# Performance work log

Measured on AMD Instinct MI355X. Metric: run time of the kernel, lower is better.

The kernel has to match this reference:

```python
import jax, jax.numpy as jnp
import numpy as np

B, C, N, K, O = 8, 64, 4096, 20, 64
EPS = 1e-5


def setup_inputs() -> dict:
    key = jax.random.key(0)
    k1, k2, k3 = jax.random.split(key, 3)
    x = jax.random.normal(k1, (B, C, N), dtype=jnp.float32)
    # Conv2d(2C, O, kernel_size=1) -> weight [O, 2C], bias [O]
    fan_in = 2 * C
    bound = 1.0 / np.sqrt(fan_in)
    W = jax.random.uniform(k2, (O, 2 * C), minval=-bound, maxval=bound, dtype=jnp.float32)
    b = jax.random.uniform(k3, (O,), minval=-bound, maxval=bound, dtype=jnp.float32)
    gamma = jnp.ones((O,), dtype=jnp.float32)
    beta = jnp.zeros((O,), dtype=jnp.float32)
    return {"x": x, "W": W, "b": b, "gamma": gamma, "beta": beta}


def reference(x, W, b, gamma, beta):
    k = K
    Bs, Cs, Ns = x.shape
    x_t = jnp.transpose(x, (0, 2, 1))  # [B, N, C]
    # pairwise squared distances (monotonic with cdist, same topk indices)
    sq = jnp.sum(x_t * x_t, axis=-1)  # [B, N]
    d2 = sq[:, :, None] + sq[:, None, :] - 2.0 * jnp.einsum("bnc,bmc->bnm", x_t, x_t)
    valid_k = min(k, Ns - 1)
    _, idx = jax.lax.top_k(-d2, valid_k + 1)  # smallest distances
    idx = idx[:, :, 1:]  # drop self -> [B, N, k]
    # gather neighbor features per batch
    nbr = jax.vmap(lambda xt, i: xt[i])(x_t, idx)  # [B, N, k, C]
    central = x_t[:, :, None, :]  # [B, N, 1, C]
    edge = jnp.concatenate(
        [jnp.broadcast_to(central, (Bs, Ns, k, Cs)), nbr - central], axis=-1
    )  # [B, N, k, 2C]
    # 1x1 conv == channel matmul
    y = jnp.einsum("bnkc,oc->bonk", edge, W) + b[None, :, None, None]  # [B, O, N, k]
    # BatchNorm2d in training mode: batch statistics over (B, N, k)
    mean = jnp.mean(y, axis=(0, 2, 3), keepdims=True)
    var = jnp.var(y, axis=(0, 2, 3), keepdims=True)
    yn = (y - mean) * jax.lax.rsqrt(var + EPS)
    yn = gamma[None, :, None, None] * yn + beta[None, :, None, None]
    out = jax.nn.relu(yn)
    return jnp.max(out, axis=-1)  # [B, O, N]
```

## Files before the change

kernel.cpp:

```cpp
#include <hip/hip_runtime.h>
#include <hip/hip_bf16.h>

#define BB 8
#define CC 64
#define NN 4096
#define KK 20
#define OO 64
#define FMAXV 3.402823466e38f

typedef __attribute__((ext_vector_type(8))) short short8;
typedef __attribute__((ext_vector_type(4))) float f32x4;

__global__ __launch_bounds__(256) void ktrans(const float* __restrict__ x,
                                              float* __restrict__ xt,
                                              unsigned short* __restrict__ xb,
                                              float* __restrict__ sq) {
  __shared__ float tile[64][65];
  const int b = blockIdx.y, n0 = blockIdx.x * 64;
  const int lane = threadIdx.x & 63, grp = threadIdx.x >> 6;
  #pragma unroll
  for (int j = 0; j < 16; ++j) {
    int c = grp + j * 4;
    tile[c][lane] = x[((size_t)b * CC + c) * NN + n0 + lane];
  }
  __syncthreads();
  #pragma unroll
  for (int j = 0; j < 16; ++j) {
    int n = grp + j * 4;
    float vv = tile[lane][n];
    size_t off = ((size_t)b * NN + n0 + n) * CC + lane;
    xt[off] = vv;
    unsigned int u = __builtin_bit_cast(unsigned int, vv);
    xb[off] = (unsigned short)((u + 0x7FFFu + ((u >> 16) & 1u)) >> 16);
  }
  if (threadIdx.x < 64) {
    float s = 0.f;
    #pragma unroll
    for (int c = 0; c < 64; ++c) { float vv = tile[c][lane]; s += vv * vv; }
    sq[(size_t)b * NN + lane + n0] = s;
  }
}

__device__ __forceinline__ int lanes_below(unsigned long long m) {
  unsigned lo = (unsigned)m, hi = (unsigned)(m >> 32);
  int c = __builtin_amdgcn_mbcnt_lo(lo, 0);
  return (int)__builtin_amdgcn_mbcnt_hi(hi, (unsigned)c);
}

__device__ __forceinline__ unsigned packkey(float d, int m) {
  unsigned u = __builtin_bit_cast(unsigned, d);
  u ^= ((int)u < 0) ? 0xFFFFFFFFu : 0x80000000u;
  return (u & 0xFFFFF000u) | (unsigned)m;
}

__device__ __forceinline__ float unpackkey(unsigned t) {
  unsigned u = t | 0xFFFu;
  u = (u & 0x80000000u) ? (u ^ 0x80000000u) : ~u;
  return __builtin_bit_cast(float, u);
}

__device__ __forceinline__ unsigned bitonic64(unsigned v, int lane) {
  #pragma unroll
  for (int k = 2; k <= 64; k <<= 1) {
    #pragma unroll
    for (int j = k >> 1; j >= 1; j >>= 1) {
      unsigned o = (unsigned)__shfl_xor((int)v, j);
      bool up    = ((lane & k) == 0);
      bool lower = ((lane & j) == 0);
      unsigned mn = (v < o) ? v : o;
      unsigned mx = (v < o) ? o : v;
      v = (up == lower) ? mn : mx;
    }
  }
  return v;
}

__global__ __launch_bounds__(256, 4) void kknn6(const unsigned short* __restrict__ xb,
                                                const float* __restrict__ sq,
                                                unsigned* __restrict__ kcand) {
  __shared__ unsigned slist[4][16][32];
  __shared__ unsigned sbuf[4][16][64];
  const int lane = threadIdx.x & 63, w = threadIdx.x >> 6;
  const int wid = blockIdx.x * 4 + w;
  const int b = wid >> 9;
  const int half = (wid >> 8) & 1;
  const int n0g = (wid & 255) * 16;
  const int ch0 = half * (NN / 2);
  const int l15 = lane & 15, q = lane >> 4;
  const unsigned long long qmask = 0xFFFFull << (q * 16);

  const unsigned short* xbB = xb + (size_t)b * NN * CC;
  const float* sqB = sq + (size_t)b * NN;

  #pragma unroll
  for (int i = 0; i < 8; ++i) {
    int idx = i * 64 + lane;
    slist[w][idx >> 5][idx & 31] = 0xFFFFFFFFu;
  }

  short8 afr[2];
  #pragma unroll
  for (int ks = 0; ks < 2; ++ks)
    afr[ks] = __builtin_bit_cast(short8, *(const int4*)(xbB + (size_t)(n0g + l15) * CC + ks * 32 + q * 8));

  float tauf4[4];
  int cnt4[4], done4[4];
  #pragma unroll
  for (int j = 0; j < 4; ++j) { tauf4[j] = FMAXV; cnt4[j] = 0; done4[j] = 0; }

  for (int t = 0; t < 32; ++t) {
    const int cb = ch0 + t * 64;
    short8 bfr[4][2];
    float sv[4];
    #pragma unroll
    for (int ct = 0; ct < 4; ++ct) {
      #pragma unroll
      for (int ks = 0; ks < 2; ++ks)
        bfr[ct][ks] = __builtin_bit_cast(short8,
            *(const int4*)(xbB + (size_t)(cb + ct * 16 + l15) * CC + ks * 32 + q * 8));
      sv[ct] = sqB[cb + ct * 16 + l15];
    }
    f32x4 acc[4];
    #pragma unroll
    for (int ct = 0; ct < 4; ++ct) {
      acc[ct] = (f32x4){0.f, 0.f, 0.f, 0.f};
      acc[ct] = __builtin_amdgcn_mfma_f32_16x16x32_bf16(afr[0], bfr[ct][0], acc[ct], 0, 0, 0);
      acc[ct] = __builtin_amdgcn_mfma_f32_16x16x32_bf16(afr[1], bfr[ct][1], acc[ct], 0, 0, 0);
    }

    #pragma unroll
    for (int ct = 0; ct < 4; ++ct) {
      const int colg = cb + ct * 16 + l15;
      float dj[4];
      bool pj[4];
      #pragma unroll
      for (int j = 0; j < 4; ++j) {
        float d = sv[ct] - 2.f * acc[ct][j];
        if (colg == n0g + q * 4 + j) d = FMAXV;
        dj[j] = d;
        pj[j] = d <= tauf4[j];
      }
      if (!__ballot(pj[0] | pj[1] | pj[2] | pj[3])) continue;
      #pragma unroll
      for (int j = 0; j < 4; ++j) {
        unsigned long long bal = __ballot(pj[j]);
        if (!bal) continue;
        const int rowl = q * 4 + j;
        int posq = lanes_below(bal & qmask);
        if (pj[j]) sbuf[w][rowl][(cnt4[j] + posq) & 63] = packkey(dj[j], colg);
        cnt4[j] += __popcll(bal & qmask);
        unsigned long long mb = __ballot(cnt4[j] - done4[j] >= 32);
        while (mb) {
          int src = __ffsll(mb) - 1;
          int qm = src >> 4;
          int rowm = qm * 4 + j;
          int dsrc = __shfl(done4[j], src);
          unsigned v = (lane < 32) ? slist[w][rowm][lane]
                                   : sbuf[w][rowm][(dsrc + lane - 32) & 63];
          v = bitonic64(v, lane);
          if (lane < 32) slist[w][rowm][lane] = v;
          unsigned tn = (unsigned)__shfl((int)v, 31);
          if (q == qm) { tauf4[j] = unpackkey(tn); done4[j] += 32; }
          mb &= ~(0xFFFFull << (qm * 16));
        }
      }
    }
  }

  #pragma unroll
  for (int j = 0; j < 4; ++j) {
    unsigned long long mb = __ballot(cnt4[j] > done4[j]);
    while (mb) {
      int src = __ffsll(mb) - 1;
      int qm = src >> 4;
      int rowm = qm * 4 + j;
      int dsrc = __shfl(done4[j], src);
      int csrc = __shfl(cnt4[j], src);
      int rem = csrc - dsrc;
      unsigned v = (lane < 32) ? slist[w][rowm][lane]
                 : ((lane - 32) < rem ? sbuf[w][rowm][(dsrc + lane - 32) & 63] : 0xFFFFFFFFu);
      v = bitonic64(v, lane);
      if (lane < 32) slist[w][rowm][lane] = v;
      if (q == qm) done4[j] = cnt4[j];
      mb &= ~(0xFFFFull << (qm * 16));
    }
  }

  unsigned* kc = kcand + (((size_t)b * 2 + half) * NN + n0g) * 32;
  #pragma unroll
  for (int i = 0; i < 8; ++i) {
    int idx = i * 64 + lane;
    kc[idx] = slist[w][idx >> 5][idx & 31];
  }
}

__global__ __launch_bounds__(256) void kmerge(const unsigned* __restrict__ kcand,
                                              const float* __restrict__ xt,
                                              const float* __restrict__ sq,
                                              int* __restrict__ knn) {
  const int lane = threadIdx.x & 63, w = threadIdx.x >> 6;
  const int gw = blockIdx.x * 4 + w;
  const int hl = lane & 31;

  for (int it = 0; it < 2; ++it) {
    const int rbase = gw * 4 + it * 2;
    const int b = rbase >> 12;
    const int n = rbase & (NN - 1);

    const unsigned* kc0 = kcand + (((size_t)b * 2 + 0) * NN) * 32;
    const unsigned* kc1 = kcand + (((size_t)b * 2 + 1) * NN) * 32;
    unsigned vA = (lane < 32) ? kc0[(size_t)n * 32 + lane] : kc1[(size_t)n * 32 + (lane - 32)];
    vA = bitonic64(vA, lane);
    unsigned vB = (lane < 32) ? kc0[(size_t)(n + 1) * 32 + lane] : kc1[(size_t)(n + 1) * 32 + (lane - 32)];
    vB = bitonic64(vB, lane);
    unsigned kx = (unsigned)__shfl_xor((int)vB, 32);
    unsigned key = (lane < 32) ? vA : kx;
    int m = (int)(key & 0xFFFu);
    const int rowg = n + ((lane >= 32) ? 1 : 0);

    const float* xtB = xt + (size_t)b * NN * CC;
    const float* sqB = sq + (size_t)b * NN;
    const float4* pr = (const float4*)(xtB + (size_t)rowg * CC);
    const float4* pm = (const float4*)(xtB + (size_t)m * CC);
    float s0 = 0.f, s1 = 0.f, s2 = 0.f, s3 = 0.f;
    #pragma unroll
    for (int i = 0; i < 16; ++i) {
      float4 a = pr[i], c = pm[i];
      s0 += a.x * c.x; s1 += a.y * c.y; s2 += a.z * c.z; s3 += a.w * c.w;
    }
    float ev = sqB[m] - 2.f * ((s0 + s1) + (s2 + s3));

    #pragma unroll
    for (int k = 2; k <= 32; k <<= 1) {
      #pragma unroll
      for (int jj = k >> 1; jj >= 1; jj >>= 1) {
        float e2 = __shfl_xor(ev, jj);
        int   m2 = __shfl_xor(m, jj);
        bool up    = ((hl & k) == 0);
        bool lower = ((hl & jj) == 0);
        bool less  = (e2 < ev) || (e2 == ev && m2 < m);
        bool take  = (up == lower) ? less : !less;
        if (take) { ev = e2; m = m2; }
      }
    }
    if (hl < KK)
      knn[((size_t)b * NN + rowg) * KK + hl] = m;
  }
}

__global__ __launch_bounds__(256) void kuv(const float* __restrict__ xt,
                                           const float* __restrict__ W,
                                           const float* __restrict__ bias,
                                           float* __restrict__ u,
                                           float* __restrict__ v) {
  __shared__ float sx[64][65];
  const int b = blockIdx.y, n0 = blockIdx.x * 64;
  const int lane = threadIdx.x & 63, w = threadIdx.x >> 6;
  const float4* src = (const float4*)(xt + ((size_t)b * NN + n0) * CC);
  for (int i = threadIdx.x; i < 1024; i += 256) {
    float4 qv = src[i];
    int nl = i >> 4, c4 = (i & 15) << 2;
    sx[nl][c4] = qv.x; sx[nl][c4+1] = qv.y; sx[nl][c4+2] = qv.z; sx[nl][c4+3] = qv.w;
  }
  const int o = lane;
  float w2r[64], wdr[64];
  const float4* W4 = (const float4*)W;
  #pragma unroll
  for (int c4 = 0; c4 < 16; ++c4) {
    float4 q1 = W4[o * 32 + c4];
    float4 q2 = W4[o * 32 + 16 + c4];
    w2r[c4*4]=q2.x; w2r[c4*4+1]=q2.y; w2r[c4*4+2]=q2.z; w2r[c4*4+3]=q2.w;
    wdr[c4*4]=q1.x-q2.x; wdr[c4*4+1]=q1.y-q2.y; wdr[c4*4+2]=q1.z-q2.z; wdr[c4*4+3]=q1.w-q2.w;
  }
  const float bo = bias[o];
  __syncthreads();
  for (int j = 0; j < 16; ++j) {
    int nl = w * 16 + j;
    float du = 0.f, dv = 0.f;
    #pragma unroll
    for (int c = 0; c < 64; ++c) {
      float xv = sx[nl][c];
      du += w2r[c] * xv;
      dv += wdr[c] * xv;
    }
    size_t off = ((size_t)b * NN + n0 + nl) * OO + o;
    u[off] = du;
    v[off] = dv + bo;
  }
}

__global__ __launch_bounds__(256) void kstats(const float* __restrict__ u,
                                              const float* __restrict__ v,
                                              const int* __restrict__ knn,
                                              float* __restrict__ umax,
                                              float* __restrict__ umin,
                                              float* __restrict__ gS) {
  const int w = threadIdx.x >> 6, lane = threadIdx.x & 63;
  const int gw = blockIdx.x * 4 + w;
  float s1 = 0.f, s2 = 0.f;
  for (int it = 0; it < 16; ++it) {
    int pair = gw * 16 + it;
    const int* ip = knn + (size_t)pair * KK;
    float vv = v[(size_t)pair * OO + lane];
    size_t ubase = ((size_t)(pair >> 12)) * NN * OO;
    float mx = -FMAXV, mn = FMAXV;
    #pragma unroll
    for (int k = 0; k < KK; ++k) {
      int id = ip[k];
      float uu = u[ubase + (size_t)id * OO + lane];
      float y = vv + uu;
      s1 += y; s2 += y * y;
      mx = fmaxf(mx, uu); mn = fminf(mn, uu);
    }
    umax[(size_t)pair * OO + lane] = mx;
    umin[(size_t)pair * OO + lane] = mn;
  }
  __shared__ float r1[4][64], r2[4][64];
  r1[w][lane] = s1; r2[w][lane] = s2;
  __syncthreads();
  if (w == 0) {
    float a = r1[0][lane] + r1[1][lane] + r1[2][lane] + r1[3][lane];
    float c = r2[0][lane] + r2[1][lane] + r2[2][lane] + r2[3][lane];
    atomicAdd(&gS[lane], a);
    atomicAdd(&gS[64 + lane], c);
  }
}

__global__ __launch_bounds__(256) void kout(const float* __restrict__ v,
                                            const float* __restrict__ umax,
                                            const float* __restrict__ umin,
                                            const float* __restrict__ gS,
                                            const float* __restrict__ gamma,
                                            const float* __restrict__ beta,
                                            float* __restrict__ out) {
  __shared__ float sA[64], sB[64];
  __shared__ float zt[64][65];
  const int b = blockIdx.y, n0 = blockIdx.x * 64;
  const int lane = threadIdx.x & 63, w = threadIdx.x >> 6;
  if (threadIdx.x < 64) {
    const float cnt = (float)BB * NN * KK;
    float m  = gS[lane] / cnt;
    float var = gS[64 + lane] / cnt - m * m;
    float A = gamma[lane] * rsqrtf(var + 1e-5f);
    sA[lane] = A;
    sB[lane] = beta[lane] - A * m;
  }
  __syncthreads();
  for (int j = 0; j < 16; ++j) {
    int nl = w * 16 + j;
    size_t off = ((size_t)b * NN + n0 + nl) * OO + lane;
    float A = sA[lane];
    float c0 = A * v[off] + sB[lane];
    float z = c0 + A * ((A > 0.f) ? umax[off] : umin[off]);
    zt[nl][lane] = fmaxf(z, 0.f);
  }
  __syncthreads();
  for (int j = 0; j < 16; ++j) {
    int o = w * 16 + j;
    out[((size_t)b * OO + o) * NN + n0 + lane] = zt[lane][o];
  }
}

extern "C" void kernel_launch(void* const* d_in, const int* in_sizes, int n_in,
                              void* d_out, int out_size, void* d_ws, size_t ws_size,
                              hipStream_t stream) {
  const float* x     = (const float*)d_in[0];
  const float* W     = (const float*)d_in[1];
  const float* bias  = (const float*)d_in[2];
  const float* gamma = (const float*)d_in[3];
  const float* beta  = (const float*)d_in[4];
  float* out = (float*)d_out;

  float* xt  = (float*)d_ws;
  float* sq  = xt  + (size_t)BB*NN*CC;
  float* u   = sq  + (size_t)BB*NN;
  float* v   = u   + (size_t)BB*NN*OO;
  float* umx = v   + (size_t)BB*NN*OO;
  float* umn = umx + (size_t)BB*NN*OO;
  float* gS  = umn + (size_t)BB*NN*OO;
  int*   knn = (int*)(gS + 128);
  unsigned short* xb = (unsigned short*)(knn + (size_t)BB*NN*KK);
  unsigned* kcand = (unsigned*)(xb + (size_t)BB*NN*CC);

  hipMemsetAsync(gS, 0, 128 * sizeof(float), stream);
  ktrans<<<dim3(NN/64, BB), 256, 0, stream>>>(x, xt, xb, sq);
  kuv   <<<dim3(NN/64, BB), 256, 0, stream>>>(xt, W, bias, u, v);
  kknn6 <<<dim3(1024),      256, 0, stream>>>(xb, sq, kcand);
  kmerge<<<dim3(2048),      256, 0, stream>>>(kcand, xt, sq, knn);
  kstats<<<dim3(512),       256, 0, stream>>>(u, v, knn, umx, umn, gS);
  kout  <<<dim3(NN/64, BB), 256, 0, stream>>>(v, umx, umn, gS, gamma, beta, out);
}
```

Baseline: 440.0 us.

## Fuse transpose with u/v projection and merge with stats; halve KNN rows per wave

```diff
diff --git a/kernel.cpp b/kernel.cpp
--- a/kernel.cpp
+++ b/kernel.cpp
@@ -11,10 +11,14 @@
 typedef __attribute__((ext_vector_type(8))) short short8;
 typedef __attribute__((ext_vector_type(4))) float f32x4;
 
-__global__ __launch_bounds__(256) void ktrans(const float* __restrict__ x,
-                                              float* __restrict__ xt,
-                                              unsigned short* __restrict__ xb,
-                                              float* __restrict__ sq) {
+__global__ __launch_bounds__(256) void kprep(const float* __restrict__ x,
+                                             const float* __restrict__ W,
+                                             const float* __restrict__ bias,
+                                             float* __restrict__ xt,
+                                             unsigned short* __restrict__ xb,
+                                             float* __restrict__ sq,
+                                             float* __restrict__ u,
+                                             float* __restrict__ v) {
   __shared__ float tile[64][65];
   const int b = blockIdx.y, n0 = blockIdx.x * 64;
   const int lane = threadIdx.x & 63, grp = threadIdx.x >> 6;
@@ -23,6 +27,16 @@
     int c = grp + j * 4;
     tile[c][lane] = x[((size_t)b * CC + c) * NN + n0 + lane];
   }
+  float w2r[64], wdr[64];
+  const float4* W4 = (const float4*)W;
+  #pragma unroll
+  for (int c4 = 0; c4 < 16; ++c4) {
+    float4 q1 = W4[lane * 32 + c4];
+    float4 q2 = W4[lane * 32 + 16 + c4];
+    w2r[c4*4]=q2.x; w2r[c4*4+1]=q2.y; w2r[c4*4+2]=q2.z; w2r[c4*4+3]=q2.w;
+    wdr[c4*4]=q1.x-q2.x; wdr[c4*4+1]=q1.y-q2.y; wdr[c4*4+2]=q1.z-q2.z; wdr[c4*4+3]=q1.w-q2.w;
+  }
+  const float bo = bias[lane];
   __syncthreads();
   #pragma unroll
   for (int j = 0; j < 16; ++j) {
@@ -30,14 +44,27 @@
     float vv = tile[lane][n];
     size_t off = ((size_t)b * NN + n0 + n) * CC + lane;
     xt[off] = vv;
-    unsigned int u = __builtin_bit_cast(unsigned int, vv);
-    xb[off] = (unsigned short)((u + 0x7FFFu + ((u >> 16) & 1u)) >> 16);
+    unsigned int uu = __builtin_bit_cast(unsigned int, vv);
+    xb[off] = (unsigned short)((uu + 0x7FFFu + ((uu >> 16) & 1u)) >> 16);
   }
   if (threadIdx.x < 64) {
     float s = 0.f;
     #pragma unroll
     for (int c = 0; c < 64; ++c) { float vv = tile[c][lane]; s += vv * vv; }
-    sq[(size_t)b * NN + lane + n0] = s;
+    sq[(size_t)b * NN + n0 + lane] = s;
+  }
+  for (int j = 0; j < 16; ++j) {
+    int nl = grp * 16 + j;
+    float du = 0.f, dv = 0.f;
+    #pragma unroll
+    for (int c = 0; c < 64; ++c) {
+      float xv = tile[c][nl];
+      du += w2r[c] * xv;
+      dv += wdr[c] * xv;
+    }
+    size_t off = ((size_t)b * NN + n0 + nl) * OO + lane;
+    u[off] = du;
+    v[off] = dv + bo;
   }
 }
 
@@ -75,25 +102,26 @@
   return v;
 }
 
-__global__ __launch_bounds__(256, 4) void kknn6(const unsigned short* __restrict__ xb,
+__global__ __launch_bounds__(256, 4) void kknn7(const unsigned short* __restrict__ xb,
                                                 const float* __restrict__ sq,
                                                 unsigned* __restrict__ kcand) {
-  __shared__ unsigned slist[4][16][32];
-  __shared__ unsigned sbuf[4][16][64];
+  __shared__ unsigned slist[4][8][32];
+  __shared__ unsigned sbuf[4][8][64];
   const int lane = threadIdx.x & 63, w = threadIdx.x >> 6;
   const int wid = blockIdx.x * 4 + w;
-  const int b = wid >> 9;
-  const int half = (wid >> 8) & 1;
-  const int n0g = (wid & 255) * 16;
+  const int b = wid >> 10;
+  const int half = (wid >> 9) & 1;
+  const int n0g = (wid & 511) * 8;
   const int ch0 = half * (NN / 2);
   const int l15 = lane & 15, q = lane >> 4;
+  const bool qlo = (q < 2);
   const unsigned long long qmask = 0xFFFFull << (q * 16);
 
   const unsigned short* xbB = xb + (size_t)b * NN * CC;
   const float* sqB = sq + (size_t)b * NN;
 
   #pragma unroll
-  for (int i = 0; i < 8; ++i) {
+  for (int i = 0; i < 4; ++i) {
     int idx = i * 64 + lane;
     slist[w][idx >> 5][idx & 31] = 0xFFFFFFFFu;
   }
@@ -101,7 +129,8 @@
   short8 afr[2];
   #pragma unroll
   for (int ks = 0; ks < 2; ++ks)
-    afr[ks] = __builtin_bit_cast(short8, *(const int4*)(xbB + (size_t)(n0g + l15) * CC + ks * 32 + q * 8));
+    afr[ks] = __builtin_bit_cast(short8,
+        *(const int4*)(xbB + (size_t)(n0g + (l15 & 7)) * CC + ks * 32 + q * 8));
 
   float tauf4[4];
   int cnt4[4], done4[4];
@@ -136,9 +165,9 @@
       #pragma unroll
       for (int j = 0; j < 4; ++j) {
         float d = sv[ct] - 2.f * acc[ct][j];
-        if (colg == n0g + q * 4 + j) d = FMAXV;
+        if (colg == n0g + ((q * 4 + j) & 7)) d = FMAXV;
         dj[j] = d;
-        pj[j] = d <= tauf4[j];
+        pj[j] = qlo && (d <= tauf4[j]);
       }
       if (!__ballot(pj[0] | pj[1] | pj[2] | pj[3])) continue;
       #pragma unroll
@@ -188,19 +217,24 @@
 
   unsigned* kc = kcand + (((size_t)b * 2 + half) * NN + n0g) * 32;
   #pragma unroll
-  for (int i = 0; i < 8; ++i) {
+  for (int i = 0; i < 4; ++i) {
     int idx = i * 64 + lane;
     kc[idx] = slist[w][idx >> 5][idx & 31];
   }
 }
 
-__global__ __launch_bounds__(256) void kmerge(const unsigned* __restrict__ kcand,
-                                              const float* __restrict__ xt,
-                                              const float* __restrict__ sq,
-                                              int* __restrict__ knn) {
+__global__ __launch_bounds__(256) void kpost(const unsigned* __restrict__ kcand,
+                                             const float* __restrict__ xt,
+                                             const float* __restrict__ sq,
+                                             const float* __restrict__ u,
+                                             const float* __restrict__ v,
+                                             float* __restrict__ umax,
+                                             float* __restrict__ umin,
+                                             float* __restrict__ gS) {
   const int lane = threadIdx.x & 63, w = threadIdx.x >> 6;
   const int gw = blockIdx.x * 4 + w;
   const int hl = lane & 31;
+  float s1 = 0.f, s2 = 0.f;
 
   for (int it = 0; it < 2; ++it) {
     const int rbase = gw * 4 + it * 2;
@@ -222,13 +256,13 @@
     const float* sqB = sq + (size_t)b * NN;
     const float4* pr = (const float4*)(xtB + (size_t)rowg * CC);
     const float4* pm = (const float4*)(xtB + (size_t)m * CC);
-    float s0 = 0.f, s1 = 0.f, s2 = 0.f, s3 = 0.f;
+    float t0 = 0.f, t1 = 0.f, t2 = 0.f, t3 = 0.f;
     #pragma unroll
     for (int i = 0; i < 16; ++i) {
       float4 a = pr[i], c = pm[i];
-      s0 += a.x * c.x; s1 += a.y * c.y; s2 += a.z * c.z; s3 += a.w * c.w;
-    }
-    float ev = sqB[m] - 2.f * ((s0 + s1) + (s2 + s3));
+      t0 += a.x * c.x; t1 += a.y * c.y; t2 += a.z * c.z; t3 += a.w * c.w;
+    }
+    float ev = sqB[m] - 2.f * ((t0 + t1) + (t2 + t3));
 
     #pragma unroll
     for (int k = 2; k <= 32; k <<= 1) {
@@ -243,86 +277,35 @@
         if (take) { ev = e2; m = m2; }
       }
     }
-    if (hl < KK)
-      knn[((size_t)b * NN + rowg) * KK + hl] = m;
-  }
-}
-
-__global__ __launch_bounds__(256) void kuv(const float* __restrict__ xt,
-                                           const float* __restrict__ W,
-                                           const float* __restrict__ bias,
-                                           float* __restrict__ u,
-                                           float* __restrict__ v) {
-  __shared__ float sx[64][65];
-  const int b = blockIdx.y, n0 = blockIdx.x * 64;
-  const int lane = threadIdx.x & 63, w = threadIdx.x >> 6;
-  const float4* src = (const float4*)(xt + ((size_t)b * NN + n0) * CC);
-  for (int i = threadIdx.x; i < 1024; i += 256) {
-    float4 qv = src[i];
-    int nl = i >> 4, c4 = (i & 15) << 2;
-    sx[nl][c4] = qv.x; sx[nl][c4+1] = qv.y; sx[nl][c4+2] = qv.z; sx[nl][c4+3] = qv.w;
-  }
-  const int o = lane;
-  float w2r[64], wdr[64];
-  const float4* W4 = (const float4*)W;
-  #pragma unroll
-  for (int c4 = 0; c4 < 16; ++c4) {
-    float4 q1 = W4[o * 32 + c4];
-    float4 q2 = W4[o * 32 + 16 + c4];
-    w2r[c4*4]=q2.x; w2r[c4*4+1]=q2.y; w2r[c4*4+2]=q2.z; w2r[c4*4+3]=q2.w;
-    wdr[c4*4]=q1.x-q2.x; wdr[c4*4+1]=q1.y-q2.y; wdr[c4*4+2]=q1.z-q2.z; wdr[c4*4+3]=q1.w-q2.w;
-  }
-  const float bo = bias[o];
-  __syncthreads();
-  for (int j = 0; j < 16; ++j) {
-    int nl = w * 16 + j;
-    float du = 0.f, dv = 0.f;
-    #pragma unroll
-    for (int c = 0; c < 64; ++c) {
-      float xv = sx[nl][c];
-      du += w2r[c] * xv;
-      dv += wdr[c] * xv;
-    }
-    size_t off = ((size_t)b * NN + n0 + nl) * OO + o;
-    u[off] = du;
-    v[off] = dv + bo;
-  }
-}
-
-__global__ __launch_bounds__(256) void kstats(const float* __restrict__ u,
-                                              const float* __restrict__ v,
-                                              const int* __restrict__ knn,
-                                              float* __restrict__ umax,
-                                              float* __restrict__ umin,
-                                              float* __restrict__ gS) {
-  const int w = threadIdx.x >> 6, lane = threadIdx.x & 63;
-  const int gw = blockIdx.x * 4 + w;
-  float s1 = 0.f, s2 = 0.f;
-  for (int it = 0; it < 16; ++it) {
-    int pair = gw * 16 + it;
-    const int* ip = knn + (size_t)pair * KK;
-    float vv = v[(size_t)pair * OO + lane];
-    size_t ubase = ((size_t)(pair >> 12)) * NN * OO;
-    float mx = -FMAXV, mn = FMAXV;
-    #pragma unroll
-    for (int k = 0; k < KK; ++k) {
-      int id = ip[k];
-      float uu = u[ubase + (size_t)id * OO + lane];
-      float y = vv + uu;
-      s1 += y; s2 += y * y;
-      mx = fmaxf(mx, uu); mn = fminf(mn, uu);
-    }
-    umax[(size_t)pair * OO + lane] = mx;
-    umin[(size_t)pair * OO + lane] = mn;
-  }
+
+    const float* uB = u + (size_t)b * NN * OO;
+    #pragma unroll
+    for (int rr = 0; rr < 2; ++rr) {
+      const int rown = n + rr;
+      float vv = v[((size_t)b * NN + rown) * OO + lane];
+      float mx = -FMAXV, mn = FMAXV;
+      #pragma unroll
+      for (int k = 0; k < KK; ++k) {
+        int id = __shfl(m, rr * 32 + k);
+        float uu = uB[(size_t)id * OO + lane];
+        float y = vv + uu;
+        s1 += y; s2 += y * y;
+        mx = fmaxf(mx, uu); mn = fminf(mn, uu);
+      }
+      umax[((size_t)b * NN + rown) * OO + lane] = mx;
+      umin[((size_t)b * NN + rown) * OO + lane] = mn;
+    }
+  }
+
   __shared__ float r1[4][64], r2[4][64];
   r1[w][lane] = s1; r2[w][lane] = s2;
   __syncthreads();
   if (w == 0) {
     float a = r1[0][lane] + r1[1][lane] + r1[2][lane] + r1[3][lane];
     float c = r2[0][lane] + r2[1][lane] + r2[2][lane] + r2[3][lane];
-    atomicAdd(&gS[lane], a);
-    atomicAdd(&gS[64 + lane], c);
+    float* g = gS + (blockIdx.x & 7) * 128;
+    atomicAdd(&g[lane], a);
+    atomicAdd(&g[64 + lane], c);
   }
 }
 
@@ -338,9 +321,15 @@
   const int b = blockIdx.y, n0 = blockIdx.x * 64;
   const int lane = threadIdx.x & 63, w = threadIdx.x >> 6;
   if (threadIdx.x < 64) {
+    float s1 = 0.f, s2 = 0.f;
+    #pragma unroll
+    for (int rsub = 0; rsub < 8; ++rsub) {
+      s1 += gS[rsub * 128 + lane];
+      s2 += gS[rsub * 128 + 64 + lane];
+    }
     const float cnt = (float)BB * NN * KK;
-    float m  = gS[lane] / cnt;
-    float var = gS[64 + lane] / cnt - m * m;
+    float m  = s1 / cnt;
+    float var = s2 / cnt - m * m;
     float A = gamma[lane] * rsqrtf(var + 1e-5f);
     sA[lane] = A;
     sB[lane] = beta[lane] - A * m;
@@ -378,15 +367,12 @@
   float* umx = v   + (size_t)BB*NN*OO;
   float* umn = umx + (size_t)BB*NN*OO;
   float* gS  = umn + (size_t)BB*NN*OO;
-  int*   knn = (int*)(gS + 128);
-  unsigned short* xb = (unsigned short*)(knn + (size_t)BB*NN*KK);
+  unsigned short* xb = (unsigned short*)(gS + 1024);
   unsigned* kcand = (unsigned*)(xb + (size_t)BB*NN*CC);
 
-  hipMemsetAsync(gS, 0, 128 * sizeof(float), stream);
-  ktrans<<<dim3(NN/64, BB), 256, 0, stream>>>(x, xt, xb, sq);
-  kuv   <<<dim3(NN/64, BB), 256, 0, stream>>>(xt, W, bias, u, v);
-  kknn6 <<<dim3(1024),      256, 0, stream>>>(xb, sq, kcand);
-  kmerge<<<dim3(2048),      256, 0, stream>>>(kcand, xt, sq, knn);
-  kstats<<<dim3(512),       256, 0, stream>>>(u, v, knn, umx, umn, gS);
-  kout  <<<dim3(NN/64, BB), 256, 0, stream>>>(v, umx, umn, gS, gamma, beta, out);
-}
+  hipMemsetAsync(gS, 0, 1024 * sizeof(float), stream);
+  kprep<<<dim3(NN/64, BB), 256, 0, stream>>>(x, W, bias, xt, xb, sq, u, v);
+  kknn7<<<dim3(2048),      256, 0, stream>>>(xb, sq, kcand);
+  kpost<<<dim3(2048),      256, 0, stream>>>(kcand, xt, sq, u, v, umx, umn, gS);
+  kout <<<dim3(NN/64, BB), 256, 0, stream>>>(v, umx, umn, gS, gamma, beta, out);
+}
```

After: 503.0 us. 14.3% more time.
